# Kernel optimization log

Hardware: AMD Instinct MI355X
Metric: run time of the kernel (lower is better)

Reference implementation:

```python
import jax, jax.numpy as jnp
import numpy as np

B, X, Y, C = 8, 64, 64, 128       # batch, spatial H, spatial W, n_channels
CTX, N, H, D = 768, 256, 8, 64    # context_dim, context len, n_heads, head_dim
HID = H * D                        # hidden_dim = 512


def _ln(x, w, b):
    # torch nn.LayerNorm: biased variance, eps=1e-5
    mu = x.mean(-1, keepdims=True)
    var = ((x - mu) ** 2).mean(-1, keepdims=True)
    return (x - mu) * jax.lax.rsqrt(var + 1e-5) * w + b


def setup_inputs() -> dict:
    key = jax.random.key(0)
    ks = jax.random.split(key, 8)
    w = lambda k, shape: jax.random.normal(k, shape, jnp.float32) * 0.02
    return {
        "xt": jax.random.normal(ks[0], (B, X, Y, C), jnp.float32),
        "context": jax.random.normal(ks[1], (B, N, CTX), jnp.float32),
        "mask": jax.random.randint(ks[2], (B, N), 0, 2).astype(bool),
        "norm_w": jnp.ones((C,), jnp.float32),
        "norm_b": jnp.zeros((C,), jnp.float32),
        "ctx_norm_w": jnp.ones((CTX,), jnp.float32),
        "ctx_norm_b": jnp.zeros((CTX,), jnp.float32),
        "Wq": w(ks[3], (C, HID)),
        "Wkv": w(ks[4], (CTX, 2 * HID)),
        "null_kv": jax.random.normal(ks[5], (2, D), jnp.float32),
        "Wout": w(ks[6], (HID, C)),
        "bout": jnp.zeros((C,), jnp.float32),
    }


def reference(xt, context, mask, norm_w, norm_b, ctx_norm_w, ctx_norm_b,
              Wq, Wkv, null_kv, Wout, bout):
    xn = _ln(xt, norm_w, norm_b)                     # [B,X,Y,C] (residual uses normed xt, as in source)
    cn = _ln(context, ctx_norm_w, ctx_norm_b)        # [B,N,CTX]

    q = (xn @ Wq).reshape(B, X * Y, H, D).transpose(0, 2, 1, 3)   # b h s d
    k, v = jnp.split(cn @ Wkv, 2, axis=-1)
    k = k.reshape(B, N, H, D).transpose(0, 2, 1, 3)               # b h n d
    v = v.reshape(B, N, H, D).transpose(0, 2, 1, 3)

    nk = jnp.broadcast_to(null_kv[0], (B, H, 1, D))
    nv = jnp.broadcast_to(null_kv[1], (B, H, 1, D))
    k = jnp.concatenate([nk, k], axis=2)                          # b h (n+1) d
    v = jnp.concatenate([nv, v], axis=2)

    scale = D ** -0.5
    sim = jnp.einsum('bhid,bhjd->bhij', q, k) * scale             # [B,H,XY,N+1]
    m = jnp.pad(mask, ((0, 0), (1, 0)), constant_values=True)[:, None, None, :]
    sim = jnp.where(m, sim, -jnp.finfo(sim.dtype).max)

    attn = jax.nn.softmax(sim.astype(jnp.float32), axis=-1)
    out = jnp.einsum('bhij,bhjd->bhid', attn, v)                  # b h s d
    out = out.transpose(0, 2, 1, 3).reshape(B, X, Y, HID)
    return out @ Wout + bout + xn
```

## Files before the change

### kernel.cpp

```cpp
#include <hip/hip_runtime.h>
#include <hip/hip_bf16.h>

typedef unsigned short u16;
typedef unsigned int u32;
typedef __attribute__((ext_vector_type(8))) __bf16 bf16x8;
typedef __attribute__((ext_vector_type(4))) float f32x4;

#define B_    8
#define S_    4096
#define C_    128
#define CTX_  768
#define N_    256
#define H_    8
#define D_    64
#define HID_  512
#define NPAD_ 320

#define QSCALE 0.1803368801111244f

#if __has_builtin(__builtin_amdgcn_exp2f)
#define EXP2(x) __builtin_amdgcn_exp2f(x)
#else
#define EXP2(x) exp2f(x)
#endif

__device__ __forceinline__ float b2f(u16 u) {
    union { u32 i; float f; } v; v.i = ((u32)u) << 16; return v.f;
}
__device__ __forceinline__ u16 f2b(float f) {
    __hip_bfloat16 h = __float2bfloat16(f);
    return *reinterpret_cast<u16*>(&h);
}
__device__ __forceinline__ bool probe_f32(const void* probe) {
    return *(const u32*)probe == 0x3F800000u;
}
__device__ __forceinline__ float ldraw(const void* p_, int i, bool f32m) {
    return f32m ? ((const float*)p_)[i] : b2f(((const u16*)p_)[i]);
}

typedef __attribute__((address_space(1))) const unsigned char gas_char;
typedef __attribute__((address_space(3))) unsigned char las_char;
__device__ __forceinline__ void gld16(const void* g, void* l) {
    __builtin_amdgcn_global_load_lds((gas_char*)g, (las_char*)l, 16, 0, 0);
}

__device__ __forceinline__ void trans64(const void* in, u16* out, int R, int Cc,
                                        int tr, int tc, bool f32m, float scale,
                                        u16 (*tile)[72]) {
    int t = threadIdx.x;
    int r = t >> 2, c4 = (t & 3) * 16;
    size_t ibase = (size_t)(tr * 64 + r) * Cc + tc * 64 + c4;
    if (f32m) {
        const float* fi = (const float*)in;
#pragma unroll
        for (int j = 0; j < 16; ++j) tile[r][c4 + j] = f2b(fi[ibase + j] * scale);
    } else {
        const u16* bi = (const u16*)in;
#pragma unroll
        for (int j = 0; j < 16; ++j) tile[r][c4 + j] = f2b(b2f(bi[ibase + j]) * scale);
    }
    __syncthreads();
    u32 wv[8];
#pragma unroll
    for (int jj = 0; jj < 8; ++jj)
        wv[jj] = (u32)tile[c4 + 2 * jj][r] | ((u32)tile[c4 + 2 * jj + 1][r] << 16);
    u16* orow = out + (size_t)(tc * 64 + r) * R + tr * 64 + c4;
    *(uint4*)orow = *(uint4*)&wv[0];
    *(uint4*)(orow + 8) = *(uint4*)&wv[4];
}

__global__ __launch_bounds__(256) void prep_ln_k(
        const void* nw, const void* nb, const void* cw, const void* cbp,
        const void* nkv, const void* bo, const void* mask_,
        const void* Wq, const void* Wkv, const void* Wout,
        const void* xt, const void* ctx,
        u16* pc, float* mb, int* posmap, int* ntarr,
        u16* WqT, u16* WkvT, u16* WoutT,
        u16* Kat, u16* Vat, u16* xn, u16* cn) {
    __shared__ __align__(16) u16 tile[64][72];
    __shared__ int wsum[4];
    bool f32m = probe_f32(nw);
    int blk = blockIdx.x, t = threadIdx.x;
    int lane = t & 63, wv = t >> 6;
    if (blk >= 8450) {
        size_t row = (size_t)(blk - 8450) * 4 + wv;
        float f[12]; float s = 0.f, sq = 0.f;
        if (f32m) {
            const float2* px = (const float2*)((const float*)ctx + row * CTX_);
#pragma unroll
            for (int i = 0; i < 6; ++i) {
                float2 v = px[lane + i * 64];
                f[2 * i] = v.x; f[2 * i + 1] = v.y; s += v.x + v.y; sq += v.x * v.x + v.y * v.y;
            }
        } else {
            const u32* px = (const u32*)((const u16*)ctx + row * CTX_);
#pragma unroll
            for (int i = 0; i < 6; ++i) {
                u32 v = px[lane + i * 64];
                float a = b2f((u16)(v & 0xffffu)), c = b2f((u16)(v >> 16));
                f[2 * i] = a; f[2 * i + 1] = c; s += a + c; sq += a * a + c * c;
            }
        }
#pragma unroll
        for (int o = 1; o < 64; o <<= 1) { s += __shfl_xor(s, o); sq += __shfl_xor(sq, o); }
        float mu = s * (1.f / CTX_), var = sq * (1.f / CTX_) - mu * mu;
        float rs = rsqrtf(var + 1e-5f);
        u32* pout = (u32*)(cn + row * CTX_);
#pragma unroll
        for (int i = 0; i < 6; ++i) {
            int col = (lane + i * 64) * 2;
            float o0 = (f[2 * i]     - mu) * rs * ldraw(cw, col, f32m)     + ldraw(cbp, col, f32m);
            float o1 = (f[2 * i + 1] - mu) * rs * ldraw(cw, col + 1, f32m) + ldraw(cbp, col + 1, f32m);
            pout[lane + i * 64] = (u32)f2b(o0) | ((u32)f2b(o1) << 16);
        }
    } else if (blk >= 258) {
        size_t row = (size_t)(blk - 258) * 4 + wv;
        float f0, f1;
        if (f32m) {
            float2 v = ((const float2*)((const float*)xt + row * C_))[lane];
            f0 = v.x; f1 = v.y;
        } else {
            u32 v = ((const u32*)((const u16*)xt + row * C_))[lane];
            f0 = b2f((u16)(v & 0xffffu)); f1 = b2f((u16)(v >> 16));
        }
        float s = f0 + f1, sq = f0 * f0 + f1 * f1;
#pragma unroll
        for (int o = 1; o < 64; o <<= 1) { s += __shfl_xor(s, o); sq += __shfl_xor(sq, o); }
        float mu = s * (1.f / C_);
        float var = sq * (1.f / C_) - mu * mu;
        float rs = rsqrtf(var + 1e-5f);
        float o0 = (f0 - mu) * rs * ldraw(nw, lane * 2, f32m)     + ldraw(nb, lane * 2, f32m);
        float o1 = (f1 - mu) * rs * ldraw(nw, lane * 2 + 1, f32m) + ldraw(nb, lane * 2 + 1, f32m);
        *(u32*)&xn[row * C_ + lane * 2] = (u32)f2b(o0) | ((u32)f2b(o1) << 16);
    } else if (blk < 8) {
        int i = blk * 256 + t;
        const void* src; int off;
        if (i < 128)       { src = nw;  off = i; }
        else if (i < 256)  { src = nb;  off = i - 128; }
        else if (i < 1024) { src = cw;  off = i - 256; }
        else if (i < 1792) { src = cbp; off = i - 1024; }
        else if (i < 1920) { src = nkv; off = i - 1792; }
        else               { src = bo;  off = i - 1920; }
        pc[i] = f2b(ldraw(src, off, f32m));
    } else if (blk < 16) {
        int b = blk - 8;
        const u32* mu = (const u32*)mask_;
        bool i32m = true;
#pragma unroll
        for (int j = 0; j < 8; ++j) i32m &= (mu[j] <= 1u);
        int m = i32m ? (((const int*)mask_)[b * N_ + t] != 0)
                     : (((const unsigned char*)mask_)[b * N_ + t] != 0);
        int v = m;
#pragma unroll
        for (int off = 1; off < 64; off <<= 1) {
            int u_ = __shfl_up(v, off);
            if (lane >= off) v += u_;
        }
        if (lane == 63) wsum[wv] = v;
        __syncthreads();
        int base = 0;
#pragma unroll
        for (int i = 0; i < 4; ++i) base += (i < wv) ? wsum[i] : 0;
        int NV = 1 + (wsum[0] + wsum[1] + wsum[2] + wsum[3]);
        posmap[b * N_ + t] = m ? (base + v) : -1;
        for (int j = t; j < NPAD_; j += 256)
            mb[b * NPAD_ + j] = (j < NV) ? 0.f : -1e30f;
        if (t == 0) ntarr[b] = (NV + 63) >> 6;
    } else if (blk < 18) {
    } else if (blk < 34) {
        int tb = blk - 18;
        trans64(Wq, WqT, C_, HID_, tb >> 3, tb & 7, f32m, QSCALE, tile);
    } else if (blk < 226) {
        int tb = blk - 34;
        trans64(Wkv, WkvT, CTX_, 2 * HID_, tb >> 4, tb & 15, f32m, 1.f, tile);
    } else if (blk < 242) {
        int tb = blk - 226;
        trans64(Wout, WoutT, HID_, C_, tb >> 1, tb & 1, f32m, 1.f, tile);
    } else {
        int idx = (blk - 242) * 256 + t;
        int d = idx & 63, bh = idx >> 6;
        Kat[(size_t)bh * NPAD_ * 64 + d] = f2b(ldraw(nkv, d, f32m));
        Vat[((size_t)bh * 64 + d) * NPAD_] = f2b(ldraw(nkv, 64 + d, f32m));
    }
}

template<int EPI, int BM, int BN>
__device__ __forceinline__ void gemm_core(
        u16* As, u16* Bs,
        const u16* __restrict__ A, const u16* __restrict__ Bt,
        int M, int N, int K, int bm, int bn,
        u16* __restrict__ out, u16* __restrict__ out2,
        const u16* __restrict__ resid, const u16* __restrict__ bias,
        const int* __restrict__ posmap, bool f32m) {
    constexpr int MR = BM / 32, NR = BN / 32;
    int tid = threadIdx.x, lane = tid & 63, w = tid >> 6;
    int wr = w >> 1, wc = w & 1;
    int rsel = lane & 15, g = lane >> 4, ksel = g * 8;
    int srow8 = lane >> 3, scol = (lane & 7) * 8;
    const u16* Ab = A + (size_t)(bm * BM) * K;
    const u16* Bb = Bt + (size_t)(bn * BN) * K;
    f32x4 acc[MR][NR] = {};
    for (int k0 = 0; k0 < K; k0 += 64) {
        if (k0) __syncthreads();
#pragma unroll
        for (int i = 0; i < BM / 32; ++i)
            gld16(Ab + (size_t)(i * 32 + w * 8 + srow8) * K + k0 + scol,
                  As + (i * 32 + w * 8) * 64);
#pragma unroll
        for (int i = 0; i < BN / 32; ++i)
            gld16(Bb + (size_t)(i * 32 + w * 8 + srow8) * K + k0 + scol,
                  Bs + (i * 32 + w * 8) * 64);
        __syncthreads();
#pragma unroll
        for (int kk = 0; kk < 2; ++kk) {
            bf16x8 af[MR], bfr[NR];
#pragma unroll
            for (int m = 0; m < MR; ++m)
                af[m] = *(const bf16x8*)&As[(wr * (BM / 2) + m * 16 + rsel) * 64 + kk * 32 + ksel];
#pragma unroll
            for (int n = 0; n < NR; ++n)
                bfr[n] = *(const bf16x8*)&Bs[(wc * (BN / 2) + n * 16 + rsel) * 64 + kk * 32 + ksel];
#pragma unroll
            for (int m = 0; m < MR; ++m)
#pragma unroll
                for (int n = 0; n < NR; ++n)
                    acc[m][n] = __builtin_amdgcn_mfma_f32_16x16x32_bf16(af[m], bfr[n], acc[m][n], 0, 0, 0);
        }
    }
#pragma unroll
    for (int m = 0; m < MR; ++m) {
#pragma unroll
        for (int n = 0; n < NR; ++n) {
            int grow0 = bm * BM + wr * (BM / 2) + m * 16 + g * 4;
            int gcol = bn * BN + wc * (BN / 2) + n * 16 + rsel;
#pragma unroll
            for (int r = 0; r < 4; ++r) {
                int grow = grow0 + r;
                float v = acc[m][n][r];
                if constexpr (EPI == 0) {
                    out[(size_t)grow * N + gcol] = f2b(v);
                } else if constexpr (EPI == 1) {
                    int bb = grow >> 8, nn = grow & 255;
                    int p_ = posmap[bb * N_ + nn];
                    if (p_ >= 0) {
                        int hh = (gcol >> 6) & 7, d = gcol & 63;
                        if (gcol < 512)
                            out[((size_t)(bb * 8 + hh) * NPAD_ + p_) * 64 + d] = f2b(v);
                        else
                            out2[((size_t)(bb * 8 + hh) * 64 + d) * NPAD_ + p_] = f2b(v);
                    }
                } else {
                    float val = v + b2f(resid[(size_t)grow * N + gcol]) + b2f(bias[gcol]);
                    if (f32m) ((float*)out)[(size_t)grow * N + gcol] = val;
                    else out[(size_t)grow * N + gcol] = f2b(val);
                }
            }
        }
    }
}

__global__ __launch_bounds__(256) void qkv_gemm_k(
        const u16* __restrict__ xn, const u16* __restrict__ WqT,
        u16* __restrict__ qbuf,
        const u16* __restrict__ cn, const u16* __restrict__ WkvT,
        u16* __restrict__ Kat, u16* __restrict__ Vat,
        const int* __restrict__ posmap) {
    __shared__ __align__(16) u16 As[128 * 64];
    __shared__ __align__(16) u16 Bs[128 * 64];
    int blk = blockIdx.x;
    if (blk < 1024) {
        int nb = ((blk & 7) << 7) + (blk >> 3);
        gemm_core<0, 128, 128>(As, Bs, xn, WqT, B_ * S_, HID_, C_,
                               nb >> 2, nb & 3, qbuf, nullptr, nullptr, nullptr,
                               nullptr, false);
    } else {
        int r = blk - 1024;
        int nr = ((r & 7) << 6) + (r >> 3);
        gemm_core<1, 64, 64>(As, Bs, cn, WkvT, B_ * N_, 2 * HID_, CTX_,
                             nr >> 4, nr & 15, Kat, Vat, nullptr, nullptr,
                             posmap, false);
    }
}

__global__ __launch_bounds__(256) void out_gemm_k(
        const u16* __restrict__ Obuf, const u16* __restrict__ WoutT,
        u16* __restrict__ out, const u16* __restrict__ xn,
        const u16* __restrict__ bias, const void* probe) {
    __shared__ __align__(16) u16 As[64 * 64];
    __shared__ __align__(16) u16 Bs[64 * 64];
    bool f32m = probe_f32(probe);
    int blk = blockIdx.x;
    int nb = ((blk & 7) << 7) + (blk >> 3);
    gemm_core<2, 64, 64>(As, Bs, Obuf, WoutT, B_ * S_, C_, HID_,
                         nb >> 1, nb & 1, out, nullptr, xn, bias,
                         nullptr, f32m);
}

__global__ __launch_bounds__(512) void attn_k(
        const u16* __restrict__ q, const u16* __restrict__ Kat,
        const u16* __restrict__ Vat, const float* __restrict__ mb,
        const int* __restrict__ ntarr, u16* __restrict__ O) {
    __shared__ __align__(16) u16 Ks[64 * 64];
    __shared__ __align__(16) u16 Vs[64 * 64];
    __shared__ __align__(16) u16 Pl[8][16 * 64];
    __shared__ __align__(16) float Bl[NPAD_];
    int tid = threadIdx.x, lane = tid & 63, w = tid >> 6;
    int nb = ((blockIdx.x & 7) << 8) + (blockIdx.x >> 3);
    int qb = nb & 31, bh = nb >> 5;
    int b = bh >> 3, h = bh & 7;
    int rsel = lane & 15, g = lane >> 4;
    int s0 = qb * 128 + w * 16;
    int swz = (rsel & 7) << 4;
    int ntb = ntarr[b];

    if (tid < NPAD_) Bl[tid] = mb[b * NPAD_ + tid];

    bf16x8 qf[2];
#pragma unroll
    for (int kk = 0; kk < 2; ++kk)
        qf[kk] = *(const bf16x8*)&q[(size_t)(b * S_ + s0 + rsel) * HID_ + h * 64 + kk * 32 + g * 8];

    const char* Kb = (const char*)(Kat + (size_t)bh * NPAD_ * 64);
    const char* Vb = (const char*)(Vat + (size_t)bh * 64 * NPAD_);
    int srow = w * 8 + (lane >> 3);
    int sbyte = (lane & 7) * 16;
    int swoff = srow * 128 + (sbyte ^ ((srow & 7) << 4));
    u16* PW = &Pl[w][0];

    f32x4 oacc[4] = {};
    float mr = -1e30f, lr = 0.f;

    uint4 kreg = *(const uint4*)(Kb + (size_t)srow * 128 + sbyte);
    uint4 vreg = *(const uint4*)(Vb + (size_t)srow * (NPAD_ * 2) + sbyte);

    for (int t = 0; t < ntb; ++t) {
        if (t) __syncthreads();
        *(uint4*)((char*)Ks + swoff) = kreg;
        *(uint4*)((char*)Vs + swoff) = vreg;
        __syncthreads();
        if (t + 1 < ntb) {
            kreg = *(const uint4*)(Kb + (size_t)((t + 1) * 64 + srow) * 128 + sbyte);
            vreg = *(const uint4*)(Vb + (size_t)srow * (NPAD_ * 2) + (t + 1) * 128 + sbyte);
        }

        f32x4 sa[4];
#pragma unroll
        for (int km = 0; km < 4; ++km)
            sa[km] = *(const f32x4*)&Bl[t * 64 + km * 16 + g * 4];
#pragma unroll
        for (int kk = 0; kk < 2; ++kk) {
#pragma unroll
            for (int km = 0; km < 4; ++km) {
                bf16x8 kf = *(const bf16x8*)((const char*)Ks
                        + (km * 16 + rsel) * 128 + ((kk * 64 + g * 16) ^ swz));
                sa[km] = __builtin_amdgcn_mfma_f32_16x16x32_bf16(kf, qf[kk], sa[km], 0, 0, 0);
            }
        }

        float sv[16];
#pragma unroll
        for (int km = 0; km < 4; ++km)
#pragma unroll
            for (int r = 0; r < 4; ++r) sv[km * 4 + r] = sa[km][r];

        float m01 = fmaxf(fmaxf(sv[0], sv[1]), fmaxf(sv[2], sv[3]));
        float m23 = fmaxf(fmaxf(sv[4], sv[5]), fmaxf(sv[6], sv[7]));
        float m45 = fmaxf(fmaxf(sv[8], sv[9]), fmaxf(sv[10], sv[11]));
        float m67 = fmaxf(fmaxf(sv[12], sv[13]), fmaxf(sv[14], sv[15]));
        float tm = fmaxf(fmaxf(m01, m23), fmaxf(m45, m67));
        tm = fmaxf(tm, __shfl_xor(tm, 16));
        tm = fmaxf(tm, __shfl_xor(tm, 32));

        if (!__all(tm <= mr + 8.f)) {
            float mn = fmaxf(mr, tm);
            float corr = EXP2(mr - mn);
            mr = mn;
            lr *= corr;
#pragma unroll
            for (int dm = 0; dm < 4; ++dm)
#pragma unroll
                for (int r = 0; r < 4; ++r) oacc[dm][r] *= corr;
        }

#pragma unroll
        for (int i = 0; i < 16; ++i) sv[i] = EXP2(sv[i] - mr);
        float s01 = (sv[0] + sv[1]) + (sv[2] + sv[3]);
        float s23 = (sv[4] + sv[5]) + (sv[6] + sv[7]);
        float s45 = (sv[8] + sv[9]) + (sv[10] + sv[11]);
        float s67 = (sv[12] + sv[13]) + (sv[14] + sv[15]);
        float ts = (s01 + s23) + (s45 + s67);
        ts += __shfl_xor(ts, 16);
        ts += __shfl_xor(ts, 32);
        lr += ts;

#pragma unroll
        for (int km = 0; km < 4; ++km) {
            uint2 pw;
            pw.x = (u32)f2b(sv[km * 4 + 0]) | ((u32)f2b(sv[km * 4 + 1]) << 16);
            pw.y = (u32)f2b(sv[km * 4 + 2]) | ((u32)f2b(sv[km * 4 + 3]) << 16);
            *(uint2*)((char*)PW + rsel * 128 + ((km * 32 + g * 8) ^ swz)) = pw;
        }

#pragma unroll
        for (int kk = 0; kk < 2; ++kk) {
            bf16x8 pb = *(const bf16x8*)((const char*)PW
                    + rsel * 128 + ((kk * 64 + g * 16) ^ swz));
#pragma unroll
            for (int dm = 0; dm < 4; ++dm) {
                bf16x8 vf = *(const bf16x8*)((const char*)Vs
                        + (dm * 16 + rsel) * 128 + ((kk * 64 + g * 16) ^ swz));
                oacc[dm] = __builtin_amdgcn_mfma_f32_16x16x32_bf16(vf, pb, oacc[dm], 0, 0, 0);
            }
        }
    }

    float inv = 1.f / lr;
#pragma unroll
    for (int dm = 0; dm < 4; ++dm) {
        uint2 pw;
        pw.x = (u32)f2b(oacc[dm][0] * inv) | ((u32)f2b(oacc[dm][1] * inv) << 16);
        pw.y = (u32)f2b(oacc[dm][2] * inv) | ((u32)f2b(oacc[dm][3] * inv) << 16);
        *(uint2*)((char*)PW + rsel * 128 + ((dm * 32 + g * 8) ^ swz)) = pw;
    }
    {
        uint4 r0 = *(const uint4*)((const char*)PW + rsel * 128 + ((g * 16) ^ swz));
        uint4 r1 = *(const uint4*)((const char*)PW + rsel * 128 + (((g + 4) * 16) ^ swz));
        char* dst = (char*)(O + (size_t)(b * S_ + s0 + rsel) * HID_ + h * 64);
        *(uint4*)(dst + g * 16) = r0;
        *(uint4*)(dst + g * 16 + 64) = r1;
    }
}

extern "C" void kernel_launch(void* const* d_in, const int* in_sizes, int n_in,
                              void* d_out, int out_size, void* d_ws, size_t ws_size,
                              hipStream_t stream) {
    const void* xt      = d_in[0];
    const void* context = d_in[1];
    const void* mask    = d_in[2];
    const void* norm_w  = d_in[3];
    const void* norm_b  = d_in[4];
    const void* cnw     = d_in[5];
    const void* cnb     = d_in[6];
    const void* Wq      = d_in[7];
    const void* Wkv     = d_in[8];
    const void* nkv     = d_in[9];
    const void* Wout    = d_in[10];
    const void* bout    = d_in[11];

    char* p = (char*)d_ws;
    u16* pc    = (u16*)p; p += 2048 * 2;
    float* mbf = (float*)p; p += (size_t)B_ * NPAD_ * 4;
    int* posmap = (int*)p; p += (size_t)B_ * N_ * 4;
    int* ntarr  = (int*)p; p += 64;
    u16* WqT   = (u16*)p; p += (size_t)HID_ * C_ * 2;
    u16* WkvT  = (u16*)p; p += (size_t)2 * HID_ * CTX_ * 2;
    u16* WoutT = (u16*)p; p += (size_t)C_ * HID_ * 2;
    u16* xn    = (u16*)p; p += (size_t)B_ * S_ * C_ * 2;
    u16* cn    = (u16*)p; p += (size_t)B_ * N_ * CTX_ * 2;
    u16* qbuf  = (u16*)p; p += (size_t)B_ * S_ * HID_ * 2;
    u16* Obuf  = (u16*)p; p += (size_t)B_ * S_ * HID_ * 2;
    u16* Kat   = (u16*)p; p += (size_t)B_ * H_ * NPAD_ * 64 * 2;
    u16* Vat   = (u16*)p; p += (size_t)B_ * H_ * 64 * NPAD_ * 2;

    prep_ln_k<<<8962, 256, 0, stream>>>(norm_w, norm_b, cnw, cnb, nkv, bout, mask,
                                        Wq, Wkv, Wout, xt, context,
                                        pc, mbf, posmap, ntarr,
                                        WqT, WkvT, WoutT, Kat, Vat, xn, cn);

    qkv_gemm_k<<<1536, 256, 0, stream>>>(xn, WqT, qbuf, cn, WkvT, Kat, Vat, posmap);

    attn_k<<<B_ * H_ * (S_ / 128), 512, 0, stream>>>(qbuf, Kat, Vat, mbf, ntarr, Obuf);

    out_gemm_k<<<1024, 256, 0, stream>>>(Obuf, WoutT, (u16*)d_out, xn, pc + 1920, norm_w);
}
```

Measured before the change: 89.98 us.

## Vectorize LayerNorm rows per sub-wave and stage out-GEMM epilogue through LDS

The xt LayerNorm now uses 16 threads per row with 8-wide vector loads and stores, and the context LayerNorm uses half-waves with 24 elements per thread, so the prep grid shrinks from 8962 to 2560 blocks. The output GEMM epilogue writes accumulators to a shared tile, then reads residual and bias with 16-byte vector loads and stores coalesced rows, replacing scattered per-element loads and stores. The aim is to cut memory transactions and block-launch overhead, at the cost of extra LDS, two barriers in the epilogue, and per-thread register pressure in the LayerNorm paths.

```diff
diff --git a/kernel.cpp b/kernel.cpp
--- a/kernel.cpp
+++ b/kernel.cpp
@@ -30,6 +30,9 @@
 __device__ __forceinline__ u16 f2b(float f) {
     __hip_bfloat16 h = __float2bfloat16(f);
     return *reinterpret_cast<u16*>(&h);
+}
+__device__ __forceinline__ u32 pk2(float a, float b) {
+    return (u32)f2b(a) | ((u32)f2b(b) << 16);
 }
 __device__ __forceinline__ bool probe_f32(const void* probe) {
     return *(const u32*)probe == 0x3F800000u;
@@ -82,56 +85,76 @@
     bool f32m = probe_f32(nw);
     int blk = blockIdx.x, t = threadIdx.x;
     int lane = t & 63, wv = t >> 6;
-    if (blk >= 8450) {
-        size_t row = (size_t)(blk - 8450) * 4 + wv;
-        float f[12]; float s = 0.f, sq = 0.f;
+    if (blk >= 2304) {
+        int l31 = lane & 31;
+        size_t row = (size_t)(blk - 2304) * 8 + wv * 2 + (lane >> 5);
+        int c0 = l31 * 24;
+        float f[24]; float s = 0.f, sq = 0.f;
         if (f32m) {
-            const float2* px = (const float2*)((const float*)ctx + row * CTX_);
+            const float4* px = (const float4*)((const float*)ctx + row * CTX_ + c0);
 #pragma unroll
             for (int i = 0; i < 6; ++i) {
-                float2 v = px[lane + i * 64];
-                f[2 * i] = v.x; f[2 * i + 1] = v.y; s += v.x + v.y; sq += v.x * v.x + v.y * v.y;
+                float4 v = px[i];
+                f[4 * i] = v.x; f[4 * i + 1] = v.y; f[4 * i + 2] = v.z; f[4 * i + 3] = v.w;
             }
         } else {
-            const u32* px = (const u32*)((const u16*)ctx + row * CTX_);
-#pragma unroll
-            for (int i = 0; i < 6; ++i) {
-                u32 v = px[lane + i * 64];
-                float a = b2f((u16)(v & 0xffffu)), c = b2f((u16)(v >> 16));
-                f[2 * i] = a; f[2 * i + 1] = c; s += a + c; sq += a * a + c * c;
-            }
-        }
-#pragma unroll
-        for (int o = 1; o < 64; o <<= 1) { s += __shfl_xor(s, o); sq += __shfl_xor(sq, o); }
+            const u16* px = (const u16*)ctx + row * CTX_ + c0;
+#pragma unroll
+            for (int i = 0; i < 3; ++i) {
+                uint4 v = *(const uint4*)&px[i * 8];
+                const u16* pv = (const u16*)&v;
+#pragma unroll
+                for (int j = 0; j < 8; ++j) f[8 * i + j] = b2f(pv[j]);
+            }
+        }
+#pragma unroll
+        for (int j = 0; j < 24; ++j) { s += f[j]; sq += f[j] * f[j]; }
+#pragma unroll
+        for (int o = 1; o < 32; o <<= 1) { s += __shfl_xor(s, o); sq += __shfl_xor(sq, o); }
         float mu = s * (1.f / CTX_), var = sq * (1.f / CTX_) - mu * mu;
         float rs = rsqrtf(var + 1e-5f);
-        u32* pout = (u32*)(cn + row * CTX_);
-#pragma unroll
-        for (int i = 0; i < 6; ++i) {
-            int col = (lane + i * 64) * 2;
-            float o0 = (f[2 * i]     - mu) * rs * ldraw(cw, col, f32m)     + ldraw(cbp, col, f32m);
-            float o1 = (f[2 * i + 1] - mu) * rs * ldraw(cw, col + 1, f32m) + ldraw(cbp, col + 1, f32m);
-            pout[lane + i * 64] = (u32)f2b(o0) | ((u32)f2b(o1) << 16);
-        }
-    } else if (blk >= 258) {
-        size_t row = (size_t)(blk - 258) * 4 + wv;
-        float f0, f1;
+        u16* pout = cn + row * CTX_ + c0;
+#pragma unroll
+        for (int i = 0; i < 3; ++i) {
+            u32 ov[4];
+#pragma unroll
+            for (int j = 0; j < 4; ++j) {
+                int e = i * 8 + j * 2;
+                float o0 = (f[e]     - mu) * rs * ldraw(cw, c0 + e, f32m)     + ldraw(cbp, c0 + e, f32m);
+                float o1 = (f[e + 1] - mu) * rs * ldraw(cw, c0 + e + 1, f32m) + ldraw(cbp, c0 + e + 1, f32m);
+                ov[j] = pk2(o0, o1);
+            }
+            *(uint4*)&pout[i * 8] = *(uint4*)ov;
+        }
+    } else if (blk >= 256) {
+        int c8 = (t & 15) * 8;
+        size_t row = (size_t)(blk - 256) * 16 + (t >> 4);
+        float f[8]; float s = 0.f, sq = 0.f;
         if (f32m) {
-            float2 v = ((const float2*)((const float*)xt + row * C_))[lane];
-            f0 = v.x; f1 = v.y;
+            const float4* px = (const float4*)((const float*)xt + row * C_ + c8);
+            float4 a = px[0], b4 = px[1];
+            f[0] = a.x; f[1] = a.y; f[2] = a.z; f[3] = a.w;
+            f[4] = b4.x; f[5] = b4.y; f[6] = b4.z; f[7] = b4.w;
         } else {
-            u32 v = ((const u32*)((const u16*)xt + row * C_))[lane];
-            f0 = b2f((u16)(v & 0xffffu)); f1 = b2f((u16)(v >> 16));
-        }
-        float s = f0 + f1, sq = f0 * f0 + f1 * f1;
-#pragma unroll
-        for (int o = 1; o < 64; o <<= 1) { s += __shfl_xor(s, o); sq += __shfl_xor(sq, o); }
-        float mu = s * (1.f / C_);
-        float var = sq * (1.f / C_) - mu * mu;
+            uint4 v = *(const uint4*)((const u16*)xt + row * C_ + c8);
+            const u16* pv = (const u16*)&v;
+#pragma unroll
+            for (int j = 0; j < 8; ++j) f[j] = b2f(pv[j]);
+        }
+#pragma unroll
+        for (int j = 0; j < 8; ++j) { s += f[j]; sq += f[j] * f[j]; }
+#pragma unroll
+        for (int o = 1; o < 16; o <<= 1) { s += __shfl_xor(s, o); sq += __shfl_xor(sq, o); }
+        float mu = s * (1.f / C_), var = sq * (1.f / C_) - mu * mu;
         float rs = rsqrtf(var + 1e-5f);
-        float o0 = (f0 - mu) * rs * ldraw(nw, lane * 2, f32m)     + ldraw(nb, lane * 2, f32m);
-        float o1 = (f1 - mu) * rs * ldraw(nw, lane * 2 + 1, f32m) + ldraw(nb, lane * 2 + 1, f32m);
-        *(u32*)&xn[row * C_ + lane * 2] = (u32)f2b(o0) | ((u32)f2b(o1) << 16);
+        u32 ov[4];
+#pragma unroll
+        for (int j = 0; j < 4; ++j) {
+            float o0 = (f[2 * j]     - mu) * rs * ldraw(nw, c8 + 2 * j, f32m)     + ldraw(nb, c8 + 2 * j, f32m);
+            float o1 = (f[2 * j + 1] - mu) * rs * ldraw(nw, c8 + 2 * j + 1, f32m) + ldraw(nb, c8 + 2 * j + 1, f32m);
+            ov[j] = pk2(o0, o1);
+        }
+        *(uint4*)&xn[row * C_ + c8] = *(uint4*)ov;
     } else if (blk < 8) {
         int i = blk * 256 + t;
         const void* src; int off;
@@ -166,18 +189,17 @@
         for (int j = t; j < NPAD_; j += 256)
             mb[b * NPAD_ + j] = (j < NV) ? 0.f : -1e30f;
         if (t == 0) ntarr[b] = (NV + 63) >> 6;
-    } else if (blk < 18) {
-    } else if (blk < 34) {
-        int tb = blk - 18;
+    } else if (blk < 32) {
+        int tb = blk - 16;
         trans64(Wq, WqT, C_, HID_, tb >> 3, tb & 7, f32m, QSCALE, tile);
-    } else if (blk < 226) {
-        int tb = blk - 34;
+    } else if (blk < 224) {
+        int tb = blk - 32;
         trans64(Wkv, WkvT, CTX_, 2 * HID_, tb >> 4, tb & 15, f32m, 1.f, tile);
-    } else if (blk < 242) {
-        int tb = blk - 226;
+    } else if (blk < 240) {
+        int tb = blk - 224;
         trans64(Wout, WoutT, HID_, C_, tb >> 1, tb & 1, f32m, 1.f, tile);
     } else {
-        int idx = (blk - 242) * 256 + t;
+        int idx = (blk - 240) * 256 + t;
         int d = idx & 63, bh = idx >> 6;
         Kat[(size_t)bh * NPAD_ * 64 + d] = f2b(ldraw(nkv, d, f32m));
         Vat[((size_t)bh * 64 + d) * NPAD_] = f2b(ldraw(nkv, 64 + d, f32m));
@@ -186,7 +208,7 @@
 
 template<int EPI, int BM, int BN>
 __device__ __forceinline__ void gemm_core(
-        u16* As, u16* Bs,
+        u16* As, u16* Bs, u16 (*T)[72],
         const u16* __restrict__ A, const u16* __restrict__ Bt,
         int M, int N, int K, int bm, int bn,
         u16* __restrict__ out, u16* __restrict__ out2,
@@ -227,6 +249,50 @@
                     acc[m][n] = __builtin_amdgcn_mfma_f32_16x16x32_bf16(af[m], bfr[n], acc[m][n], 0, 0, 0);
         }
     }
+    if constexpr (EPI == 2) {
+        __syncthreads();
+#pragma unroll
+        for (int m = 0; m < MR; ++m)
+#pragma unroll
+            for (int n = 0; n < NR; ++n) {
+                int trow = wr * (BM / 2) + m * 16 + g * 4;
+                int tcol = wc * (BN / 2) + n * 16 + rsel;
+#pragma unroll
+                for (int r = 0; r < 4; ++r)
+                    T[trow + r][tcol] = f2b(acc[m][n][r]);
+            }
+        __syncthreads();
+        int row = tid >> 2, cst = (tid & 3) * 16;
+        int grow = bm * BM + row, gcol0 = bn * BN + cst;
+        uint4 tv0 = *(const uint4*)&T[row][cst];
+        uint4 tv1 = *(const uint4*)&T[row][cst + 8];
+        uint4 rv0 = *(const uint4*)&resid[(size_t)grow * N + gcol0];
+        uint4 rv1 = *(const uint4*)&resid[(size_t)grow * N + gcol0 + 8];
+        uint4 bv0 = *(const uint4*)&bias[gcol0];
+        uint4 bv1 = *(const uint4*)&bias[gcol0 + 8];
+        const u16* tp = (const u16*)&tv0;
+        const u16* rp = (const u16*)&rv0;
+        const u16* bp = (const u16*)&bv0;
+        float o[16];
+#pragma unroll
+        for (int j = 0; j < 8; ++j) o[j] = b2f(tp[j]) + b2f(rp[j]) + b2f(bp[j]);
+        tp = (const u16*)&tv1; rp = (const u16*)&rv1; bp = (const u16*)&bv1;
+#pragma unroll
+        for (int j = 0; j < 8; ++j) o[8 + j] = b2f(tp[j]) + b2f(rp[j]) + b2f(bp[j]);
+        if (f32m) {
+            float* po = (float*)out + (size_t)grow * N + gcol0;
+#pragma unroll
+            for (int j = 0; j < 16; ++j) po[j] = o[j];
+        } else {
+            u32 ov[8];
+#pragma unroll
+            for (int j = 0; j < 8; ++j) ov[j] = pk2(o[2 * j], o[2 * j + 1]);
+            u16* po = out + (size_t)grow * N + gcol0;
+            *(uint4*)po = *(uint4*)&ov[0];
+            *(uint4*)(po + 8) = *(uint4*)&ov[4];
+        }
+        return;
+    }
 #pragma unroll
     for (int m = 0; m < MR; ++m) {
 #pragma unroll
@@ -249,10 +315,6 @@
                         else
                             out2[((size_t)(bb * 8 + hh) * 64 + d) * NPAD_ + p_] = f2b(v);
                     }
-                } else {
-                    float val = v + b2f(resid[(size_t)grow * N + gcol]) + b2f(bias[gcol]);
-                    if (f32m) ((float*)out)[(size_t)grow * N + gcol] = val;
-                    else out[(size_t)grow * N + gcol] = f2b(val);
                 }
             }
         }
@@ -270,13 +332,13 @@
     int blk = blockIdx.x;
     if (blk < 1024) {
         int nb = ((blk & 7) << 7) + (blk >> 3);
-        gemm_core<0, 128, 128>(As, Bs, xn, WqT, B_ * S_, HID_, C_,
+        gemm_core<0, 128, 128>(As, Bs, nullptr, xn, WqT, B_ * S_, HID_, C_,
                                nb >> 2, nb & 3, qbuf, nullptr, nullptr, nullptr,
                                nullptr, false);
     } else {
         int r = blk - 1024;
         int nr = ((r & 7) << 6) + (r >> 3);
-        gemm_core<1, 64, 64>(As, Bs, cn, WkvT, B_ * N_, 2 * HID_, CTX_,
+        gemm_core<1, 64, 64>(As, Bs, nullptr, cn, WkvT, B_ * N_, 2 * HID_, CTX_,
                              nr >> 4, nr & 15, Kat, Vat, nullptr, nullptr,
                              posmap, false);
     }
@@ -288,10 +350,11 @@
         const u16* __restrict__ bias, const void* probe) {
     __shared__ __align__(16) u16 As[64 * 64];
     __shared__ __align__(16) u16 Bs[64 * 64];
+    __shared__ __align__(16) u16 T[64][72];
     bool f32m = probe_f32(probe);
     int blk = blockIdx.x;
     int nb = ((blk & 7) << 7) + (blk >> 3);
-    gemm_core<2, 64, 64>(As, Bs, Obuf, WoutT, B_ * S_, C_, HID_,
+    gemm_core<2, 64, 64>(As, Bs, T, Obuf, WoutT, B_ * S_, C_, HID_,
                          nb >> 1, nb & 1, out, nullptr, xn, bias,
                          nullptr, f32m);
 }
@@ -396,8 +459,8 @@
 #pragma unroll
         for (int km = 0; km < 4; ++km) {
             uint2 pw;
-            pw.x = (u32)f2b(sv[km * 4 + 0]) | ((u32)f2b(sv[km * 4 + 1]) << 16);
-            pw.y = (u32)f2b(sv[km * 4 + 2]) | ((u32)f2b(sv[km * 4 + 3]) << 16);
+            pw.x = pk2(sv[km * 4 + 0], sv[km * 4 + 1]);
+            pw.y = pk2(sv[km * 4 + 2], sv[km * 4 + 3]);
             *(uint2*)((char*)PW + rsel * 128 + ((km * 32 + g * 8) ^ swz)) = pw;
         }
 
@@ -418,8 +481,8 @@
 #pragma unroll
     for (int dm = 0; dm < 4; ++dm) {
         uint2 pw;
-        pw.x = (u32)f2b(oacc[dm][0] * inv) | ((u32)f2b(oacc[dm][1] * inv) << 16);
-        pw.y = (u32)f2b(oacc[dm][2] * inv) | ((u32)f2b(oacc[dm][3] * inv) << 16);
+        pw.x = pk2(oacc[dm][0] * inv, oacc[dm][1] * inv);
+        pw.y = pk2(oacc[dm][2] * inv, oacc[dm][3] * inv);
         *(uint2*)((char*)PW + rsel * 128 + ((dm * 32 + g * 8) ^ swz)) = pw;
     }
     {
@@ -462,7 +525,7 @@
     u16* Kat   = (u16*)p; p += (size_t)B_ * H_ * NPAD_ * 64 * 2;
     u16* Vat   = (u16*)p; p += (size_t)B_ * H_ * 64 * NPAD_ * 2;
 
-    prep_ln_k<<<8962, 256, 0, stream>>>(norm_w, norm_b, cnw, cnb, nkv, bout, mask,
+    prep_ln_k<<<2560, 256, 0, stream>>>(norm_w, norm_b, cnw, cnb, nkv, bout, mask,
                                         Wq, Wkv, Wout, xt, context,
                                         pc, mbf, posmap, ntarr,
                                         WqT, WkvT, WoutT, Kat, Vat, xn, cn);
```

Result: slower. 102.2 us (+13.6%).
